# Optimization experiments

Measured on AMD Instinct MI355X. Metric: run time of the kernel, lower is better.

The kernel has to match this reference:

```python
import jax, jax.numpy as jnp
import numpy as np

HIDDEN = 2048
NUM_HEADS = 16
HEAD_DIM = 128
WINDOW_SIZE = 512
NUM_GLOBAL = 16
SCALING = HEAD_DIM ** -0.5


def setup_inputs() -> dict:
    key = jax.random.key(0)
    ks = jax.random.split(key, 5)
    std = HIDDEN ** -0.5
    hidden_states = jax.random.normal(ks[0], (1, 4096, HIDDEN), dtype=jnp.float32)
    # Linear weights stored as (in, out) so y = x @ W
    Wq = jax.random.normal(ks[1], (HIDDEN, NUM_HEADS * HEAD_DIM), dtype=jnp.float32) * std
    Wk = jax.random.normal(ks[2], (HIDDEN, NUM_HEADS * HEAD_DIM), dtype=jnp.float32) * std
    Wv = jax.random.normal(ks[3], (HIDDEN, NUM_HEADS * HEAD_DIM), dtype=jnp.float32) * std
    Wo = jax.random.normal(ks[4], (NUM_HEADS * HEAD_DIM, HIDDEN), dtype=jnp.float32) * std
    return {"hidden_states": hidden_states, "Wq": Wq, "Wk": Wk, "Wv": Wv, "Wo": Wo}


def _sliding_mask(q_len: int, kv_len: int) -> jnp.ndarray:
    q_pos = jnp.arange(q_len)[:, None]
    kv_pos = jnp.arange(kv_len)[None, :]
    half_window = WINDOW_SIZE // 2
    local = jnp.abs(q_pos - kv_pos) < half_window
    glob = (q_pos < NUM_GLOBAL) | (kv_pos < NUM_GLOBAL)
    mask = local | glob
    return jnp.where(mask, 0.0, -jnp.inf).astype(jnp.float32)


def reference(hidden_states, Wq, Wk, Wv, Wo):
    bsz, q_len, _ = hidden_states.shape
    q = (hidden_states @ Wq).reshape(bsz, q_len, NUM_HEADS, HEAD_DIM).transpose(0, 2, 1, 3)
    k = (hidden_states @ Wk).reshape(bsz, q_len, NUM_HEADS, HEAD_DIM).transpose(0, 2, 1, 3)
    v = (hidden_states @ Wv).reshape(bsz, q_len, NUM_HEADS, HEAD_DIM).transpose(0, 2, 1, 3)
    mask = _sliding_mask(q_len, q_len)[None, None]  # [1,1,S,S]
    scores = jnp.einsum("bhqd,bhkd->bhqk", q, k) * SCALING + mask
    attn = jax.nn.softmax(scores.astype(jnp.float32), axis=-1).astype(q.dtype)
    out = jnp.einsum("bhqk,bhkd->bhqd", attn, v)
    out = out.transpose(0, 2, 1, 3).reshape(bsz, q_len, NUM_HEADS * HEAD_DIM)
    return out @ Wo
```

## Files before the change

### kernel.cpp

```cpp
#include <hip/hip_runtime.h>
#include <stdint.h>

#define SEQ    4096
#define HID    2048
#define NQKV   6144
#define QKW    4096
#define NH     16
#define HD     128
#define SCALE  0.08838834764831845f
#define GQC    32

typedef unsigned short u16;
typedef __attribute__((ext_vector_type(8))) short bf16x8;
typedef __attribute__((ext_vector_type(4))) float f32x4;

__device__ __forceinline__ u16 f2bf(float f) {
  union { float f; unsigned u; } v; v.f = f;
  unsigned r = v.u + 0x7FFFu + ((v.u >> 16) & 1u);
  return (u16)(r >> 16);
}

__device__ __forceinline__ float bf2f(u16 b) {
  union { unsigned u; float f; } c; c.u = ((unsigned)b) << 16; return c.f;
}

__device__ __forceinline__ void async16(const u16* g, u16* l) {
  __builtin_amdgcn_global_load_lds(
      (const __attribute__((address_space(1))) unsigned int*)g,
      (__attribute__((address_space(3))) unsigned int*)l, 16, 0, 0);
}

__global__ __launch_bounds__(256) void cvt_f32_bf16(const float* __restrict__ in,
                                                    u16* __restrict__ out, int n4) {
  int i = blockIdx.x * 256 + threadIdx.x;
  if (i >= n4) return;
  float4 v = ((const float4*)in)[i];
  ushort4 o;
  o.x = f2bf(v.x); o.y = f2bf(v.y); o.z = f2bf(v.z); o.w = f2bf(v.w);
  ((ushort4*)out)[i] = o;
}

__global__ __launch_bounds__(256) void transpose_w4(const float* __restrict__ W0,
                                                    const float* __restrict__ W1,
                                                    const float* __restrict__ W2,
                                                    const float* __restrict__ W3,
                                                    u16* __restrict__ Wcat,
                                                    u16* __restrict__ Wot) {
  __shared__ __align__(16) u16 Ts[64 * 68];
  const int n0 = blockIdx.x * 64;
  const int k0 = blockIdx.y * 64;
  const int z = blockIdx.z;
  const float* W = (z == 0) ? W0 : (z == 1) ? W1 : (z == 2) ? W2 : W3;
  u16* Wt = (z < 3) ? (Wcat + (size_t)z * 2048 * 2048) : Wot;
  const int t = threadIdx.x;
#pragma unroll
  for (int p = 0; p < 4; ++p) {
    int f = (t + p * 256) * 4;
    int r = f >> 6, c = f & 63;
    float4 v = *(const float4*)&W[(size_t)(k0 + r) * 2048 + n0 + c];
    ushort4 o; o.x = f2bf(v.x); o.y = f2bf(v.y); o.z = f2bf(v.z); o.w = f2bf(v.w);
    *(ushort4*)&Ts[r * 68 + c] = o;
  }
  __syncthreads();
#pragma unroll
  for (int p = 0; p < 4; ++p) {
    int g = (t + p * 256) * 4;
    int r = g >> 6, c = g & 63;
    ushort4 o;
    o.x = Ts[(c + 0) * 68 + r];
    o.y = Ts[(c + 1) * 68 + r];
    o.z = Ts[(c + 2) * 68 + r];
    o.w = Ts[(c + 3) * 68 + r];
    *(ushort4*)&Wt[(size_t)(n0 + r) * 2048 + k0 + c] = o;
  }
}

template <typename OutT, bool WVT>
__global__ __launch_bounds__(256) void gemm_bt(const u16* __restrict__ A,
                                               const u16* __restrict__ B,
                                               OutT* __restrict__ C,
                                               u16* __restrict__ VTout,
                                               int K, int ldc) {
  __shared__ __align__(16) u16 As[128 * 32];
  __shared__ __align__(16) u16 Bs[128 * 32];
  const int m0 = blockIdx.y * 128;
  const int n0 = blockIdx.x * 128;
  const int tid = threadIdx.x;
  const int wid = tid >> 6;
  const int lane = tid & 63;
  const int wm = wid & 1, wn = wid >> 1;
  const int l15 = lane & 15, g4 = lane >> 4;

  const int srow = wid * 32 + (lane >> 2);
  const int scol = (lane & 3) * 8;

  f32x4 acc[4][4] = {};

  const u16* pa0 = &A[(size_t)(m0 + srow) * K + scol];
  const u16* pa1 = &A[(size_t)(m0 + srow + 16) * K + scol];
  const u16* pb0 = &B[(size_t)(n0 + srow) * K + scol];
  const u16* pb1 = &B[(size_t)(n0 + srow + 16) * K + scol];
  u16* la0 = &As[(wid * 32) * 32];
  u16* la1 = &As[(wid * 32 + 16) * 32];
  u16* lb0 = &Bs[(wid * 32) * 32];
  u16* lb1 = &Bs[(wid * 32 + 16) * 32];

  for (int kt = 0; kt < K; kt += 32) {
    __syncthreads();
    async16(pa0 + kt, la0);
    async16(pa1 + kt, la1);
    async16(pb0 + kt, lb0);
    async16(pb1 + kt, lb1);
    __syncthreads();
    bf16x8 af[4], bfr[4];
#pragma unroll
    for (int i = 0; i < 4; ++i)
      af[i] = *(const bf16x8*)&As[(wm * 64 + i * 16 + l15) * 32 + g4 * 8];
#pragma unroll
    for (int i = 0; i < 4; ++i)
      bfr[i] = *(const bf16x8*)&Bs[(wn * 64 + i * 16 + l15) * 32 + g4 * 8];
#pragma unroll
    for (int mi = 0; mi < 4; ++mi)
#pragma unroll
      for (int ni = 0; ni < 4; ++ni)
        acc[mi][ni] = __builtin_amdgcn_mfma_f32_16x16x32_bf16(af[mi], bfr[ni], acc[mi][ni], 0, 0, 0);
  }

  if (WVT && n0 >= QKW) {
#pragma unroll
    for (int mi = 0; mi < 4; ++mi)
#pragma unroll
      for (int ni = 0; ni < 4; ++ni) {
        const int nv = n0 - QKW + wn * 64 + ni * 16 + l15;
        const int hh = nv >> 7, dd = nv & 127;
        u16* base = &VTout[((size_t)hh * HD + dd) * SEQ];
        const int mb = m0 + wm * 64 + mi * 16 + g4 * 4;
        u16 pk[4];
#pragma unroll
        for (int r = 0; r < 4; ++r) pk[r] = f2bf(acc[mi][ni][r]);
        *(uint2*)&base[mb] = *(uint2*)pk;
      }
  } else {
#pragma unroll
    for (int mi = 0; mi < 4; ++mi)
#pragma unroll
      for (int ni = 0; ni < 4; ++ni) {
        const int n = n0 + wn * 64 + ni * 16 + l15;
#pragma unroll
        for (int r = 0; r < 4; ++r) {
          const int m = m0 + wm * 64 + mi * 16 + g4 * 4 + r;
          float v = acc[mi][ni][r];
          if constexpr (sizeof(OutT) == 2) {
            C[(size_t)m * ldc + n] = (OutT)f2bf(v);
          } else {
            C[(size_t)m * ldc + n] = v;
          }
        }
      }
  }
}

__global__ __launch_bounds__(256, 2) void attn_kernel(const u16* __restrict__ qk,
                                                      const u16* __restrict__ vt,
                                                      u16* __restrict__ out) {
  __shared__ __align__(16) u16 Ks[64 * 128];
  __shared__ __align__(16) u16 VTs[128 * 64];
  __shared__ __align__(16) u16 Ps[128 * 64];
  const int q0 = blockIdx.x * 128;
  const int h = blockIdx.y;
  const int tid = threadIdx.x;
  const int w = tid >> 6;
  const int lane = tid & 63;
  const int l15 = lane & 15, g4 = lane >> 4, l7 = lane & 7;

  bf16x8 qf[2][4];
#pragma unroll
  for (int qs = 0; qs < 2; ++qs) {
    const u16* qrow = &qk[(size_t)(q0 + w * 32 + qs * 16 + l15) * QKW + h * HD + g4 * 8];
#pragma unroll
    for (int kk = 0; kk < 4; ++kk) qf[qs][kk] = *(const bf16x8*)&qrow[kk * 32];
  }

  float m_run[2] = {-1e30f, -1e30f}, l_run[2] = {0.f, 0.f};
  f32x4 o[2][8] = {};

  int lo = q0 - 255;
  int lo_blk = (lo < 0) ? 0 : (lo >> 6);
  int hi_blk = (q0 + 382) >> 6;
  if (hi_blk > 63) hi_blk = 63;
  const int extra = (lo_blk > 0) ? 1 : 0;
  const int nsteps = hi_blk - lo_blk + 1 + extra;

  for (int step = 0; step < nsteps; ++step) {
    const int kb = (extra && step == 0) ? 0 : (lo_blk + step - extra);
    const int kv0 = kb * 64;
    __syncthreads();
#pragma unroll
    for (int p = 0; p < 4; ++p) {
      const int r = w * 16 + p * 4 + (lane >> 4);
      const u16* src = &qk[(size_t)(kv0 + r) * QKW + 2048 + h * HD + (((lane & 15) ^ (r & 15)) * 8)];
      async16(src, &Ks[(w * 16 + p * 4) * 128]);
    }
#pragma unroll
    for (int p = 0; p < 4; ++p) {
      const int r = w * 32 + p * 8 + (lane >> 3);
      const u16* src = &vt[(size_t)h * (HD * SEQ) + (size_t)r * SEQ + kv0 + (((lane & 7) ^ (r & 7)) * 8)];
      async16(src, &VTs[(w * 32 + p * 8) * 64]);
    }
    __syncthreads();

    f32x4 st[2][4] = {};
#pragma unroll
    for (int kk = 0; kk < 4; ++kk) {
      bf16x8 ak[4];
#pragma unroll
      for (int t4 = 0; t4 < 4; ++t4)
        ak[t4] = *(const bf16x8*)&Ks[(t4 * 16 + l15) * 128 + (((kk * 4 + g4) ^ l15) * 8)];
#pragma unroll
      for (int qs = 0; qs < 2; ++qs)
#pragma unroll
        for (int t4 = 0; t4 < 4; ++t4)
          st[qs][t4] = __builtin_amdgcn_mfma_f32_16x16x32_bf16(ak[t4], qf[qs][kk], st[qs][t4], 0, 0, 0);
    }

#pragma unroll
    for (int qs = 0; qs < 2; ++qs) {
      const int q = q0 + w * 32 + qs * 16 + l15;
      float cmax = -1e30f;
#pragma unroll
      for (int t4 = 0; t4 < 4; ++t4)
#pragma unroll
        for (int r = 0; r < 4; ++r) {
          int kv = kv0 + t4 * 16 + g4 * 4 + r;
          int dq = q - kv; if (dq < 0) dq = -dq;
          bool ok = (dq < 256) || (kv < 16);
          float s = ok ? st[qs][t4][r] * SCALE : -1e30f;
          st[qs][t4][r] = s;
          cmax = fmaxf(cmax, s);
        }
      cmax = fmaxf(cmax, __shfl_xor(cmax, 16, 64));
      cmax = fmaxf(cmax, __shfl_xor(cmax, 32, 64));
      float mnew = fmaxf(m_run[qs], cmax);
      float csum = 0.f;
#pragma unroll
      for (int t4 = 0; t4 < 4; ++t4)
#pragma unroll
        for (int r = 0; r < 4; ++r) {
          float p = __expf(st[qs][t4][r] - mnew);
          st[qs][t4][r] = p;
          csum += p;
        }
      csum += __shfl_xor(csum, 16, 64);
      csum += __shfl_xor(csum, 32, 64);
      float a = __expf(m_run[qs] - mnew);
      m_run[qs] = mnew;
      l_run[qs] = l_run[qs] * a + csum;

#pragma unroll
      for (int t4 = 0; t4 < 4; ++t4) {
        u16 pk[4];
#pragma unroll
        for (int r = 0; r < 4; ++r) pk[r] = f2bf(st[qs][t4][r]);
        int c8 = t4 * 2 + (g4 >> 1);
        *(uint2*)&Ps[(w * 32 + qs * 16 + l15) * 64 + ((c8 ^ l7) * 8) + (g4 & 1) * 4] = *(uint2*)pk;
      }
#pragma unroll
      for (int nt = 0; nt < 8; ++nt)
#pragma unroll
        for (int r = 0; r < 4; ++r) o[qs][nt][r] *= a;
    }

#pragma unroll
    for (int ks = 0; ks < 2; ++ks) {
      bf16x8 ap[2];
#pragma unroll
      for (int qs = 0; qs < 2; ++qs)
        ap[qs] = *(const bf16x8*)&Ps[(w * 32 + qs * 16 + l15) * 64 + (((ks * 4 + g4) ^ l7) * 8)];
#pragma unroll
      for (int nt = 0; nt < 8; ++nt) {
        bf16x8 bv = *(const bf16x8*)&VTs[(nt * 16 + l15) * 64 + (((ks * 4 + g4) ^ l7) * 8)];
#pragma unroll
        for (int qs = 0; qs < 2; ++qs)
          o[qs][nt] = __builtin_amdgcn_mfma_f32_16x16x32_bf16(bv, ap[qs], o[qs][nt], 0, 0, 0);
      }
    }
  }

#pragma unroll
  for (int qs = 0; qs < 2; ++qs) {
    if (q0 + w * 32 + qs * 16 < 16) continue;
    const int q = q0 + w * 32 + qs * 16 + l15;
    const float inv = 1.f / l_run[qs];
#pragma unroll
    for (int nt = 0; nt < 8; ++nt) {
      u16 pk[4];
#pragma unroll
      for (int r = 0; r < 4; ++r) pk[r] = f2bf(o[qs][nt][r] * inv);
      *(uint2*)&out[(size_t)q * HID + h * HD + nt * 16 + g4 * 4] = *(uint2*)pk;
    }
  }
}

__global__ __launch_bounds__(256) void attn_global(const u16* __restrict__ qk,
                                                   const u16* __restrict__ vt,
                                                   float* __restrict__ Opart,
                                                   float* __restrict__ MLpart) {
  __shared__ __align__(16) u16 Ks[64 * 136];
  __shared__ __align__(16) u16 Vs[64 * 136];
  const int chunk = blockIdx.x, h = blockIdx.y;
  const int t = threadIdx.x;
  const int q = t >> 4, dg = t & 15;

  float qr[8];
  {
    bf16x8 v = *(const bf16x8*)&qk[(size_t)q * QKW + h * HD + dg * 8];
#pragma unroll
    for (int j = 0; j < 8; ++j) qr[j] = bf2f((u16)v[j]);
  }
  float m_run = -1e30f, l_run = 0.f, o[8] = {};
  const int kvbase = chunk * (SEQ / GQC);

  for (int st = 0; st < (SEQ / GQC) / 64; ++st) {
    const int kv0 = kvbase + st * 64;
    __syncthreads();
#pragma unroll
    for (int p = 0; p < 4; ++p) {
      int f = (t + p * 256) * 8;
      int r = f >> 7, c = f & 127;
      *(uint4*)&Ks[r * 136 + c] = *(const uint4*)&qk[(size_t)(kv0 + r) * QKW + 2048 + h * HD + c];
    }
#pragma unroll
    for (int p = 0; p < 4; ++p) {
      int id = p * 256 + t;
      int d = id >> 3, c8 = id & 7;
      uint4 v = *(const uint4*)&vt[(size_t)h * (HD * SEQ) + (size_t)d * SEQ + kv0 + c8 * 8];
      const u16* pv16 = (const u16*)&v;
#pragma unroll
      for (int j = 0; j < 8; ++j) Vs[(c8 * 8 + j) * 136 + d] = pv16[j];
    }
    __syncthreads();
    for (int kv = 0; kv < 64; ++kv) {
      bf16x8 kr = *(const bf16x8*)&Ks[kv * 136 + dg * 8];
      float s = 0.f;
#pragma unroll
      for (int j = 0; j < 8; ++j) s += qr[j] * bf2f((u16)kr[j]);
      s += __shfl_xor(s, 1, 64); s += __shfl_xor(s, 2, 64);
      s += __shfl_xor(s, 4, 64); s += __shfl_xor(s, 8, 64);
      s *= SCALE;
      float mnew = fmaxf(m_run, s);
      float alpha = __expf(m_run - mnew);
      float p = __expf(s - mnew);
      m_run = mnew;
      l_run = l_run * alpha + p;
      bf16x8 vr = *(const bf16x8*)&Vs[kv * 136 + dg * 8];
#pragma unroll
      for (int j = 0; j < 8; ++j) o[j] = o[j] * alpha + p * bf2f((u16)vr[j]);
    }
  }
  float* op = &Opart[(((size_t)h * GQC + chunk) * 16 + q) * HD + dg * 8];
#pragma unroll
  for (int j = 0; j < 8; ++j) op[j] = o[j];
  if (dg == 0) {
    float* ml = &MLpart[(((size_t)h * GQC + chunk) * 16 + q) * 2];
    ml[0] = m_run; ml[1] = l_run;
  }
}

__global__ __launch_bounds__(256) void attn_gred(const float* __restrict__ Opart,
                                                 const float* __restrict__ MLpart,
                                                 u16* __restrict__ out) {
  const int h = blockIdx.x;
  const int t = threadIdx.x;
  const int q = t >> 4, dg = t & 15;
  float M = -1e30f;
  for (int c = 0; c < GQC; ++c)
    M = fmaxf(M, MLpart[(((size_t)h * GQC + c) * 16 + q) * 2]);
  float L = 0.f, o[8] = {};
  for (int c = 0; c < GQC; ++c) {
    const float* ml = &MLpart[(((size_t)h * GQC + c) * 16 + q) * 2];
    float e = __expf(ml[0] - M);
    L += e * ml[1];
    const float* op = &Opart[(((size_t)h * GQC + c) * 16 + q) * HD + dg * 8];
#pragma unroll
    for (int j = 0; j < 8; ++j) o[j] += e * op[j];
  }
  float inv = 1.f / L;
  u16 tmp[8];
#pragma unroll
  for (int j = 0; j < 8; ++j) tmp[j] = f2bf(o[j] * inv);
  *(uint4*)&out[(size_t)q * HID + h * HD + dg * 8] = *(uint4*)tmp;
}

extern "C" void kernel_launch(void* const* d_in, const int* in_sizes, int n_in,
                              void* d_out, int out_size, void* d_ws, size_t ws_size,
                              hipStream_t stream) {
  const float* X  = (const float*)d_in[0];
  const float* Wq = (const float*)d_in[1];
  const float* Wk = (const float*)d_in[2];
  const float* Wv = (const float*)d_in[3];
  const float* Wo = (const float*)d_in[4];
  float* out = (float*)d_out;

  char* ws = (char*)d_ws;
  u16* Xbf    = (u16*)(ws);
  u16* Wcat   = (u16*)(ws + (size_t)(16 << 20));
  u16* AttnO  = (u16*)(ws + (size_t)(16 << 20));
  float* Opart  = (float*)(ws + (size_t)(32 << 20));
  float* MLpart = (float*)(ws + (size_t)(36 << 20));
  u16* QK     = (u16*)(ws + (size_t)(40 << 20));
  u16* VT     = (u16*)(ws + (size_t)(72 << 20));
  u16* Wot    = (u16*)(ws + (size_t)(88 << 20));

  cvt_f32_bf16<<<dim3(8192), dim3(256), 0, stream>>>(X, Xbf, (SEQ * HID) / 4);
  transpose_w4<<<dim3(32, 32, 4), 256, 0, stream>>>(Wq, Wk, Wv, Wo, Wcat, Wot);
  gemm_bt<u16, true><<<dim3(48, 32), 256, 0, stream>>>(Xbf, Wcat, QK, VT, HID, QKW);
  attn_global<<<dim3(GQC, NH), 256, 0, stream>>>(QK, VT, Opart, MLpart);
  attn_kernel<<<dim3(SEQ / 128, NH), 256, 0, stream>>>(QK, VT, AttnO);
  attn_gred<<<dim3(NH), 256, 0, stream>>>(Opart, MLpart, AttnO);
  gemm_bt<float, false><<<dim3(16, 32), 256, 0, stream>>>(AttnO, Wot, out, nullptr, HID, HID);
}
```

Before: 431.2 us.

## Merge prep kernels, fuse attention launches with atomic reduction, double K-step in GEMM

```diff
diff --git a/kernel.cpp b/kernel.cpp
--- a/kernel.cpp
+++ b/kernel.cpp
@@ -30,29 +30,33 @@
       (__attribute__((address_space(3))) unsigned int*)l, 16, 0, 0);
 }
 
-__global__ __launch_bounds__(256) void cvt_f32_bf16(const float* __restrict__ in,
-                                                    u16* __restrict__ out, int n4) {
-  int i = blockIdx.x * 256 + threadIdx.x;
-  if (i >= n4) return;
-  float4 v = ((const float4*)in)[i];
-  ushort4 o;
-  o.x = f2bf(v.x); o.y = f2bf(v.y); o.z = f2bf(v.z); o.w = f2bf(v.w);
-  ((ushort4*)out)[i] = o;
-}
-
-__global__ __launch_bounds__(256) void transpose_w4(const float* __restrict__ W0,
-                                                    const float* __restrict__ W1,
-                                                    const float* __restrict__ W2,
-                                                    const float* __restrict__ W3,
-                                                    u16* __restrict__ Wcat,
-                                                    u16* __restrict__ Wot) {
+__global__ __launch_bounds__(256) void prep(const float* __restrict__ X,
+                                            const float* __restrict__ W0,
+                                            const float* __restrict__ W1,
+                                            const float* __restrict__ W2,
+                                            const float* __restrict__ W3,
+                                            u16* __restrict__ Xbf,
+                                            u16* __restrict__ Wcat,
+                                            u16* __restrict__ Wot,
+                                            unsigned* __restrict__ cnt) {
+  const int bx = blockIdx.x;
+  const int t = threadIdx.x;
+  if (bx == 0 && t < NH) cnt[t] = 0u;
+  if (bx < 8192) {
+    int i = bx * 256 + t;
+    float4 v = ((const float4*)X)[i];
+    ushort4 o;
+    o.x = f2bf(v.x); o.y = f2bf(v.y); o.z = f2bf(v.z); o.w = f2bf(v.w);
+    ((ushort4*)Xbf)[i] = o;
+    return;
+  }
   __shared__ __align__(16) u16 Ts[64 * 68];
-  const int n0 = blockIdx.x * 64;
-  const int k0 = blockIdx.y * 64;
-  const int z = blockIdx.z;
+  const int b = bx - 8192;
+  const int z = b >> 10;
+  const int k0 = ((b >> 5) & 31) * 64;
+  const int n0 = (b & 31) * 64;
   const float* W = (z == 0) ? W0 : (z == 1) ? W1 : (z == 2) ? W2 : W3;
   u16* Wt = (z < 3) ? (Wcat + (size_t)z * 2048 * 2048) : Wot;
-  const int t = threadIdx.x;
 #pragma unroll
   for (int p = 0; p < 4; ++p) {
     int f = (t + p * 256) * 4;
@@ -81,8 +85,10 @@
                                                OutT* __restrict__ C,
                                                u16* __restrict__ VTout,
                                                int K, int ldc) {
-  __shared__ __align__(16) u16 As[128 * 32];
-  __shared__ __align__(16) u16 Bs[128 * 32];
+  __shared__ __align__(16) u16 As0[128 * 32];
+  __shared__ __align__(16) u16 As1[128 * 32];
+  __shared__ __align__(16) u16 Bs0[128 * 32];
+  __shared__ __align__(16) u16 Bs1[128 * 32];
   const int m0 = blockIdx.y * 128;
   const int n0 = blockIdx.x * 128;
   const int tid = threadIdx.x;
@@ -100,30 +106,47 @@
   const u16* pa1 = &A[(size_t)(m0 + srow + 16) * K + scol];
   const u16* pb0 = &B[(size_t)(n0 + srow) * K + scol];
   const u16* pb1 = &B[(size_t)(n0 + srow + 16) * K + scol];
-  u16* la0 = &As[(wid * 32) * 32];
-  u16* la1 = &As[(wid * 32 + 16) * 32];
-  u16* lb0 = &Bs[(wid * 32) * 32];
-  u16* lb1 = &Bs[(wid * 32 + 16) * 32];
-
-  for (int kt = 0; kt < K; kt += 32) {
+  const int lo0 = (wid * 32) * 32, lo1 = (wid * 32 + 16) * 32;
+
+  for (int kt = 0; kt < K; kt += 64) {
     __syncthreads();
-    async16(pa0 + kt, la0);
-    async16(pa1 + kt, la1);
-    async16(pb0 + kt, lb0);
-    async16(pb1 + kt, lb1);
+    async16(pa0 + kt, &As0[lo0]);
+    async16(pa1 + kt, &As0[lo1]);
+    async16(pb0 + kt, &Bs0[lo0]);
+    async16(pb1 + kt, &Bs0[lo1]);
+    async16(pa0 + kt + 32, &As1[lo0]);
+    async16(pa1 + kt + 32, &As1[lo1]);
+    async16(pb0 + kt + 32, &Bs1[lo0]);
+    async16(pb1 + kt + 32, &Bs1[lo1]);
     __syncthreads();
-    bf16x8 af[4], bfr[4];
-#pragma unroll
-    for (int i = 0; i < 4; ++i)
-      af[i] = *(const bf16x8*)&As[(wm * 64 + i * 16 + l15) * 32 + g4 * 8];
-#pragma unroll
-    for (int i = 0; i < 4; ++i)
-      bfr[i] = *(const bf16x8*)&Bs[(wn * 64 + i * 16 + l15) * 32 + g4 * 8];
-#pragma unroll
-    for (int mi = 0; mi < 4; ++mi)
-#pragma unroll
-      for (int ni = 0; ni < 4; ++ni)
-        acc[mi][ni] = __builtin_amdgcn_mfma_f32_16x16x32_bf16(af[mi], bfr[ni], acc[mi][ni], 0, 0, 0);
+    {
+      bf16x8 af[4], bfr[4];
+#pragma unroll
+      for (int i = 0; i < 4; ++i)
+        af[i] = *(const bf16x8*)&As0[(wm * 64 + i * 16 + l15) * 32 + g4 * 8];
+#pragma unroll
+      for (int i = 0; i < 4; ++i)
+        bfr[i] = *(const bf16x8*)&Bs0[(wn * 64 + i * 16 + l15) * 32 + g4 * 8];
+#pragma unroll
+      for (int mi = 0; mi < 4; ++mi)
+#pragma unroll
+        for (int ni = 0; ni < 4; ++ni)
+          acc[mi][ni] = __builtin_amdgcn_mfma_f32_16x16x32_bf16(af[mi], bfr[ni], acc[mi][ni], 0, 0, 0);
+    }
+    {
+      bf16x8 af[4], bfr[4];
+#pragma unroll
+      for (int i = 0; i < 4; ++i)
+        af[i] = *(const bf16x8*)&As1[(wm * 64 + i * 16 + l15) * 32 + g4 * 8];
+#pragma unroll
+      for (int i = 0; i < 4; ++i)
+        bfr[i] = *(const bf16x8*)&Bs1[(wn * 64 + i * 16 + l15) * 32 + g4 * 8];
+#pragma unroll
+      for (int mi = 0; mi < 4; ++mi)
+#pragma unroll
+        for (int ni = 0; ni < 4; ++ni)
+          acc[mi][ni] = __builtin_amdgcn_mfma_f32_16x16x32_bf16(af[mi], bfr[ni], acc[mi][ni], 0, 0, 0);
+    }
   }
 
   if (WVT && n0 >= QKW) {
@@ -160,235 +183,243 @@
   }
 }
 
-__global__ __launch_bounds__(256, 2) void attn_kernel(const u16* __restrict__ qk,
-                                                      const u16* __restrict__ vt,
-                                                      u16* __restrict__ out) {
-  __shared__ __align__(16) u16 Ks[64 * 128];
-  __shared__ __align__(16) u16 VTs[128 * 64];
-  __shared__ __align__(16) u16 Ps[128 * 64];
-  const int q0 = blockIdx.x * 128;
+__global__ __launch_bounds__(256, 2) void attn_fused(const u16* __restrict__ qk,
+                                                     const u16* __restrict__ vt,
+                                                     u16* __restrict__ out,
+                                                     float* __restrict__ Opart,
+                                                     float* __restrict__ MLpart,
+                                                     unsigned* __restrict__ cnt) {
+  __shared__ __align__(16) u16 smem[24576];
+  __shared__ unsigned lastflag;
   const int h = blockIdx.y;
   const int tid = threadIdx.x;
-  const int w = tid >> 6;
   const int lane = tid & 63;
-  const int l15 = lane & 15, g4 = lane >> 4, l7 = lane & 7;
-
-  bf16x8 qf[2][4];
-#pragma unroll
-  for (int qs = 0; qs < 2; ++qs) {
-    const u16* qrow = &qk[(size_t)(q0 + w * 32 + qs * 16 + l15) * QKW + h * HD + g4 * 8];
-#pragma unroll
-    for (int kk = 0; kk < 4; ++kk) qf[qs][kk] = *(const bf16x8*)&qrow[kk * 32];
-  }
-
-  float m_run[2] = {-1e30f, -1e30f}, l_run[2] = {0.f, 0.f};
-  f32x4 o[2][8] = {};
-
-  int lo = q0 - 255;
-  int lo_blk = (lo < 0) ? 0 : (lo >> 6);
-  int hi_blk = (q0 + 382) >> 6;
-  if (hi_blk > 63) hi_blk = 63;
-  const int extra = (lo_blk > 0) ? 1 : 0;
-  const int nsteps = hi_blk - lo_blk + 1 + extra;
-
-  for (int step = 0; step < nsteps; ++step) {
-    const int kb = (extra && step == 0) ? 0 : (lo_blk + step - extra);
-    const int kv0 = kb * 64;
+
+  if (blockIdx.x < 32) {
+    u16* Ks  = smem;
+    u16* VTs = smem + 8192;
+    u16* Ps  = smem + 16384;
+    const int q0 = blockIdx.x * 128;
+    const int w = tid >> 6;
+    const int l15 = lane & 15, g4 = lane >> 4, l7 = lane & 7;
+
+    bf16x8 qf[2][4];
+#pragma unroll
+    for (int qs = 0; qs < 2; ++qs) {
+      const u16* qrow = &qk[(size_t)(q0 + w * 32 + qs * 16 + l15) * QKW + h * HD + g4 * 8];
+#pragma unroll
+      for (int kk = 0; kk < 4; ++kk) qf[qs][kk] = *(const bf16x8*)&qrow[kk * 32];
+    }
+
+    float m_run[2] = {-1e30f, -1e30f}, l_run[2] = {0.f, 0.f};
+    f32x4 o[2][8] = {};
+
+    int lo = q0 - 255;
+    int lo_blk = (lo < 0) ? 0 : (lo >> 6);
+    int hi_blk = (q0 + 382) >> 6;
+    if (hi_blk > 63) hi_blk = 63;
+    const int extra = (lo_blk > 0) ? 1 : 0;
+    const int nsteps = hi_blk - lo_blk + 1 + extra;
+
+    for (int step = 0; step < nsteps; ++step) {
+      const int kb = (extra && step == 0) ? 0 : (lo_blk + step - extra);
+      const int kv0 = kb * 64;
+      __syncthreads();
+#pragma unroll
+      for (int p = 0; p < 4; ++p) {
+        const int r = w * 16 + p * 4 + (lane >> 4);
+        const u16* src = &qk[(size_t)(kv0 + r) * QKW + 2048 + h * HD + (((lane & 15) ^ (r & 15)) * 8)];
+        async16(src, &Ks[(w * 16 + p * 4) * 128]);
+      }
+#pragma unroll
+      for (int p = 0; p < 4; ++p) {
+        const int r = w * 32 + p * 8 + (lane >> 3);
+        const u16* src = &vt[(size_t)h * (HD * SEQ) + (size_t)r * SEQ + kv0 + (((lane & 7) ^ (r & 7)) * 8)];
+        async16(src, &VTs[(w * 32 + p * 8) * 64]);
+      }
+      __syncthreads();
+
+      f32x4 st[2][4] = {};
+#pragma unroll
+      for (int kk = 0; kk < 4; ++kk) {
+        bf16x8 ak[4];
+#pragma unroll
+        for (int t4 = 0; t4 < 4; ++t4)
+          ak[t4] = *(const bf16x8*)&Ks[(t4 * 16 + l15) * 128 + (((kk * 4 + g4) ^ l15) * 8)];
+#pragma unroll
+        for (int qs = 0; qs < 2; ++qs)
+#pragma unroll
+          for (int t4 = 0; t4 < 4; ++t4)
+            st[qs][t4] = __builtin_amdgcn_mfma_f32_16x16x32_bf16(ak[t4], qf[qs][kk], st[qs][t4], 0, 0, 0);
+      }
+
+#pragma unroll
+      for (int qs = 0; qs < 2; ++qs) {
+        const int q = q0 + w * 32 + qs * 16 + l15;
+        float cmax = -1e30f;
+#pragma unroll
+        for (int t4 = 0; t4 < 4; ++t4)
+#pragma unroll
+          for (int r = 0; r < 4; ++r) {
+            int kv = kv0 + t4 * 16 + g4 * 4 + r;
+            int dq = q - kv; if (dq < 0) dq = -dq;
+            bool ok = (dq < 256) || (kv < 16);
+            float s = ok ? st[qs][t4][r] * SCALE : -1e30f;
+            st[qs][t4][r] = s;
+            cmax = fmaxf(cmax, s);
+          }
+        cmax = fmaxf(cmax, __shfl_xor(cmax, 16, 64));
+        cmax = fmaxf(cmax, __shfl_xor(cmax, 32, 64));
+        float mnew = fmaxf(m_run[qs], cmax);
+        float csum = 0.f;
+#pragma unroll
+        for (int t4 = 0; t4 < 4; ++t4)
+#pragma unroll
+          for (int r = 0; r < 4; ++r) {
+            float p = __expf(st[qs][t4][r] - mnew);
+            st[qs][t4][r] = p;
+            csum += p;
+          }
+        csum += __shfl_xor(csum, 16, 64);
+        csum += __shfl_xor(csum, 32, 64);
+        float a = __expf(m_run[qs] - mnew);
+        m_run[qs] = mnew;
+        l_run[qs] = l_run[qs] * a + csum;
+
+#pragma unroll
+        for (int t4 = 0; t4 < 4; ++t4) {
+          u16 pk[4];
+#pragma unroll
+          for (int r = 0; r < 4; ++r) pk[r] = f2bf(st[qs][t4][r]);
+          int c8 = t4 * 2 + (g4 >> 1);
+          *(uint2*)&Ps[(w * 32 + qs * 16 + l15) * 64 + ((c8 ^ l7) * 8) + (g4 & 1) * 4] = *(uint2*)pk;
+        }
+#pragma unroll
+        for (int nt = 0; nt < 8; ++nt)
+#pragma unroll
+          for (int r = 0; r < 4; ++r) o[qs][nt][r] *= a;
+      }
+
+#pragma unroll
+      for (int ks = 0; ks < 2; ++ks) {
+        bf16x8 ap[2];
+#pragma unroll
+        for (int qs = 0; qs < 2; ++qs)
+          ap[qs] = *(const bf16x8*)&Ps[(w * 32 + qs * 16 + l15) * 64 + (((ks * 4 + g4) ^ l7) * 8)];
+#pragma unroll
+        for (int nt = 0; nt < 8; ++nt) {
+          bf16x8 bv = *(const bf16x8*)&VTs[(nt * 16 + l15) * 64 + (((ks * 4 + g4) ^ l7) * 8)];
+#pragma unroll
+          for (int qs = 0; qs < 2; ++qs)
+            o[qs][nt] = __builtin_amdgcn_mfma_f32_16x16x32_bf16(bv, ap[qs], o[qs][nt], 0, 0, 0);
+        }
+      }
+    }
+
+#pragma unroll
+    for (int qs = 0; qs < 2; ++qs) {
+      if (q0 + w * 32 + qs * 16 < 16) continue;
+      const int q = q0 + w * 32 + qs * 16 + l15;
+      const float inv = 1.f / l_run[qs];
+#pragma unroll
+      for (int nt = 0; nt < 8; ++nt) {
+        u16 pk[4];
+#pragma unroll
+        for (int r = 0; r < 4; ++r) pk[r] = f2bf(o[qs][nt][r] * inv);
+        *(uint2*)&out[(size_t)q * HID + h * HD + nt * 16 + g4 * 4] = *(uint2*)pk;
+      }
+    }
+    return;
+  }
+
+  {
+    u16* Ks = smem;
+    u16* Vs = smem + 8704;
+    const int chunk = blockIdx.x - 32;
+    const int t = tid;
+    const int q = t >> 4, dg = t & 15;
+
+    float qr[8];
+    {
+      bf16x8 v = *(const bf16x8*)&qk[(size_t)q * QKW + h * HD + dg * 8];
+#pragma unroll
+      for (int j = 0; j < 8; ++j) qr[j] = bf2f((u16)v[j]);
+    }
+    float m_run = -1e30f, l_run = 0.f, o[8] = {};
+    const int kvbase = chunk * (SEQ / GQC);
+
+    for (int st = 0; st < (SEQ / GQC) / 64; ++st) {
+      const int kv0 = kvbase + st * 64;
+      __syncthreads();
+#pragma unroll
+      for (int p = 0; p < 4; ++p) {
+        int f = (t + p * 256) * 8;
+        int r = f >> 7, c = f & 127;
+        *(uint4*)&Ks[r * 136 + c] = *(const uint4*)&qk[(size_t)(kv0 + r) * QKW + 2048 + h * HD + c];
+      }
+#pragma unroll
+      for (int p = 0; p < 4; ++p) {
+        int id = p * 256 + t;
+        int d = id >> 3, c8 = id & 7;
+        uint4 v = *(const uint4*)&vt[(size_t)h * (HD * SEQ) + (size_t)d * SEQ + kv0 + c8 * 8];
+        const u16* pv16 = (const u16*)&v;
+#pragma unroll
+        for (int j = 0; j < 8; ++j) Vs[(c8 * 8 + j) * 136 + d] = pv16[j];
+      }
+      __syncthreads();
+      for (int kv = 0; kv < 64; ++kv) {
+        bf16x8 kr = *(const bf16x8*)&Ks[kv * 136 + dg * 8];
+        float s = 0.f;
+#pragma unroll
+        for (int j = 0; j < 8; ++j) s += qr[j] * bf2f((u16)kr[j]);
+        s += __shfl_xor(s, 1, 64); s += __shfl_xor(s, 2, 64);
+        s += __shfl_xor(s, 4, 64); s += __shfl_xor(s, 8, 64);
+        s *= SCALE;
+        float mnew = fmaxf(m_run, s);
+        float alpha = __expf(m_run - mnew);
+        float p = __expf(s - mnew);
+        m_run = mnew;
+        l_run = l_run * alpha + p;
+        bf16x8 vr = *(const bf16x8*)&Vs[kv * 136 + dg * 8];
+#pragma unroll
+        for (int j = 0; j < 8; ++j) o[j] = o[j] * alpha + p * bf2f((u16)vr[j]);
+      }
+    }
+    float* op = &Opart[(((size_t)h * GQC + chunk) * 16 + q) * HD + dg * 8];
+#pragma unroll
+    for (int j = 0; j < 8; ++j) op[j] = o[j];
+    if (dg == 0) {
+      float* ml = &MLpart[(((size_t)h * GQC + chunk) * 16 + q) * 2];
+      ml[0] = m_run; ml[1] = l_run;
+    }
+
     __syncthreads();
-#pragma unroll
-    for (int p = 0; p < 4; ++p) {
-      const int r = w * 16 + p * 4 + (lane >> 4);
-      const u16* src = &qk[(size_t)(kv0 + r) * QKW + 2048 + h * HD + (((lane & 15) ^ (r & 15)) * 8)];
-      async16(src, &Ks[(w * 16 + p * 4) * 128]);
-    }
-#pragma unroll
-    for (int p = 0; p < 4; ++p) {
-      const int r = w * 32 + p * 8 + (lane >> 3);
-      const u16* src = &vt[(size_t)h * (HD * SEQ) + (size_t)r * SEQ + kv0 + (((lane & 7) ^ (r & 7)) * 8)];
-      async16(src, &VTs[(w * 32 + p * 8) * 64]);
+    if (t == 0) {
+      __threadfence();
+      lastflag = (atomicAdd(&cnt[h], 1u) == GQC - 1) ? 1u : 0u;
     }
     __syncthreads();
-
-    f32x4 st[2][4] = {};
-#pragma unroll
-    for (int kk = 0; kk < 4; ++kk) {
-      bf16x8 ak[4];
-#pragma unroll
-      for (int t4 = 0; t4 < 4; ++t4)
-        ak[t4] = *(const bf16x8*)&Ks[(t4 * 16 + l15) * 128 + (((kk * 4 + g4) ^ l15) * 8)];
-#pragma unroll
-      for (int qs = 0; qs < 2; ++qs)
-#pragma unroll
-        for (int t4 = 0; t4 < 4; ++t4)
-          st[qs][t4] = __builtin_amdgcn_mfma_f32_16x16x32_bf16(ak[t4], qf[qs][kk], st[qs][t4], 0, 0, 0);
-    }
-
-#pragma unroll
-    for (int qs = 0; qs < 2; ++qs) {
-      const int q = q0 + w * 32 + qs * 16 + l15;
-      float cmax = -1e30f;
-#pragma unroll
-      for (int t4 = 0; t4 < 4; ++t4)
-#pragma unroll
-        for (int r = 0; r < 4; ++r) {
-          int kv = kv0 + t4 * 16 + g4 * 4 + r;
-          int dq = q - kv; if (dq < 0) dq = -dq;
-          bool ok = (dq < 256) || (kv < 16);
-          float s = ok ? st[qs][t4][r] * SCALE : -1e30f;
-          st[qs][t4][r] = s;
-          cmax = fmaxf(cmax, s);
-        }
-      cmax = fmaxf(cmax, __shfl_xor(cmax, 16, 64));
-      cmax = fmaxf(cmax, __shfl_xor(cmax, 32, 64));
-      float mnew = fmaxf(m_run[qs], cmax);
-      float csum = 0.f;
-#pragma unroll
-      for (int t4 = 0; t4 < 4; ++t4)
-#pragma unroll
-        for (int r = 0; r < 4; ++r) {
-          float p = __expf(st[qs][t4][r] - mnew);
-          st[qs][t4][r] = p;
-          csum += p;
-        }
-      csum += __shfl_xor(csum, 16, 64);
-      csum += __shfl_xor(csum, 32, 64);
-      float a = __expf(m_run[qs] - mnew);
-      m_run[qs] = mnew;
-      l_run[qs] = l_run[qs] * a + csum;
-
-#pragma unroll
-      for (int t4 = 0; t4 < 4; ++t4) {
-        u16 pk[4];
-#pragma unroll
-        for (int r = 0; r < 4; ++r) pk[r] = f2bf(st[qs][t4][r]);
-        int c8 = t4 * 2 + (g4 >> 1);
-        *(uint2*)&Ps[(w * 32 + qs * 16 + l15) * 64 + ((c8 ^ l7) * 8) + (g4 & 1) * 4] = *(uint2*)pk;
-      }
-#pragma unroll
-      for (int nt = 0; nt < 8; ++nt)
-#pragma unroll
-        for (int r = 0; r < 4; ++r) o[qs][nt][r] *= a;
-    }
-
-#pragma unroll
-    for (int ks = 0; ks < 2; ++ks) {
-      bf16x8 ap[2];
-#pragma unroll
-      for (int qs = 0; qs < 2; ++qs)
-        ap[qs] = *(const bf16x8*)&Ps[(w * 32 + qs * 16 + l15) * 64 + (((ks * 4 + g4) ^ l7) * 8)];
-#pragma unroll
-      for (int nt = 0; nt < 8; ++nt) {
-        bf16x8 bv = *(const bf16x8*)&VTs[(nt * 16 + l15) * 64 + (((ks * 4 + g4) ^ l7) * 8)];
-#pragma unroll
-        for (int qs = 0; qs < 2; ++qs)
-          o[qs][nt] = __builtin_amdgcn_mfma_f32_16x16x32_bf16(bv, ap[qs], o[qs][nt], 0, 0, 0);
-      }
-    }
-  }
-
-#pragma unroll
-  for (int qs = 0; qs < 2; ++qs) {
-    if (q0 + w * 32 + qs * 16 < 16) continue;
-    const int q = q0 + w * 32 + qs * 16 + l15;
-    const float inv = 1.f / l_run[qs];
-#pragma unroll
-    for (int nt = 0; nt < 8; ++nt) {
-      u16 pk[4];
-#pragma unroll
-      for (int r = 0; r < 4; ++r) pk[r] = f2bf(o[qs][nt][r] * inv);
-      *(uint2*)&out[(size_t)q * HID + h * HD + nt * 16 + g4 * 4] = *(uint2*)pk;
-    }
-  }
-}
-
-__global__ __launch_bounds__(256) void attn_global(const u16* __restrict__ qk,
-                                                   const u16* __restrict__ vt,
-                                                   float* __restrict__ Opart,
-                                                   float* __restrict__ MLpart) {
-  __shared__ __align__(16) u16 Ks[64 * 136];
-  __shared__ __align__(16) u16 Vs[64 * 136];
-  const int chunk = blockIdx.x, h = blockIdx.y;
-  const int t = threadIdx.x;
-  const int q = t >> 4, dg = t & 15;
-
-  float qr[8];
-  {
-    bf16x8 v = *(const bf16x8*)&qk[(size_t)q * QKW + h * HD + dg * 8];
-#pragma unroll
-    for (int j = 0; j < 8; ++j) qr[j] = bf2f((u16)v[j]);
-  }
-  float m_run = -1e30f, l_run = 0.f, o[8] = {};
-  const int kvbase = chunk * (SEQ / GQC);
-
-  for (int st = 0; st < (SEQ / GQC) / 64; ++st) {
-    const int kv0 = kvbase + st * 64;
-    __syncthreads();
-#pragma unroll
-    for (int p = 0; p < 4; ++p) {
-      int f = (t + p * 256) * 8;
-      int r = f >> 7, c = f & 127;
-      *(uint4*)&Ks[r * 136 + c] = *(const uint4*)&qk[(size_t)(kv0 + r) * QKW + 2048 + h * HD + c];
-    }
-#pragma unroll
-    for (int p = 0; p < 4; ++p) {
-      int id = p * 256 + t;
-      int d = id >> 3, c8 = id & 7;
-      uint4 v = *(const uint4*)&vt[(size_t)h * (HD * SEQ) + (size_t)d * SEQ + kv0 + c8 * 8];
-      const u16* pv16 = (const u16*)&v;
-#pragma unroll
-      for (int j = 0; j < 8; ++j) Vs[(c8 * 8 + j) * 136 + d] = pv16[j];
-    }
-    __syncthreads();
-    for (int kv = 0; kv < 64; ++kv) {
-      bf16x8 kr = *(const bf16x8*)&Ks[kv * 136 + dg * 8];
-      float s = 0.f;
-#pragma unroll
-      for (int j = 0; j < 8; ++j) s += qr[j] * bf2f((u16)kr[j]);
-      s += __shfl_xor(s, 1, 64); s += __shfl_xor(s, 2, 64);
-      s += __shfl_xor(s, 4, 64); s += __shfl_xor(s, 8, 64);
-      s *= SCALE;
-      float mnew = fmaxf(m_run, s);
-      float alpha = __expf(m_run - mnew);
-      float p = __expf(s - mnew);
-      m_run = mnew;
-      l_run = l_run * alpha + p;
-      bf16x8 vr = *(const bf16x8*)&Vs[kv * 136 + dg * 8];
-#pragma unroll
-      for (int j = 0; j < 8; ++j) o[j] = o[j] * alpha + p * bf2f((u16)vr[j]);
-    }
-  }
-  float* op = &Opart[(((size_t)h * GQC + chunk) * 16 + q) * HD + dg * 8];
-#pragma unroll
-  for (int j = 0; j < 8; ++j) op[j] = o[j];
-  if (dg == 0) {
-    float* ml = &MLpart[(((size_t)h * GQC + chunk) * 16 + q) * 2];
-    ml[0] = m_run; ml[1] = l_run;
-  }
-}
-
-__global__ __launch_bounds__(256) void attn_gred(const float* __restrict__ Opart,
-                                                 const float* __restrict__ MLpart,
-                                                 u16* __restrict__ out) {
-  const int h = blockIdx.x;
-  const int t = threadIdx.x;
-  const int q = t >> 4, dg = t & 15;
-  float M = -1e30f;
-  for (int c = 0; c < GQC; ++c)
-    M = fmaxf(M, MLpart[(((size_t)h * GQC + c) * 16 + q) * 2]);
-  float L = 0.f, o[8] = {};
-  for (int c = 0; c < GQC; ++c) {
-    const float* ml = &MLpart[(((size_t)h * GQC + c) * 16 + q) * 2];
-    float e = __expf(ml[0] - M);
-    L += e * ml[1];
-    const float* op = &Opart[(((size_t)h * GQC + c) * 16 + q) * HD + dg * 8];
-#pragma unroll
-    for (int j = 0; j < 8; ++j) o[j] += e * op[j];
-  }
-  float inv = 1.f / L;
-  u16 tmp[8];
-#pragma unroll
-  for (int j = 0; j < 8; ++j) tmp[j] = f2bf(o[j] * inv);
-  *(uint4*)&out[(size_t)q * HID + h * HD + dg * 8] = *(uint4*)tmp;
+    if (lastflag) {
+      __threadfence();
+      float M = -1e30f;
+      for (int c = 0; c < GQC; ++c)
+        M = fmaxf(M, MLpart[(((size_t)h * GQC + c) * 16 + q) * 2]);
+      float L = 0.f, oo[8] = {};
+      for (int c = 0; c < GQC; ++c) {
+        const float* ml = &MLpart[(((size_t)h * GQC + c) * 16 + q) * 2];
+        float e = __expf(ml[0] - M);
+        L += e * ml[1];
+        const float* opc = &Opart[(((size_t)h * GQC + c) * 16 + q) * HD + dg * 8];
+#pragma unroll
+        for (int j = 0; j < 8; ++j) oo[j] += e * opc[j];
+      }
+      float inv = 1.f / L;
+      u16 tmp[8];
+#pragma unroll
+      for (int j = 0; j < 8; ++j) tmp[j] = f2bf(oo[j] * inv);
+      *(uint4*)&out[(size_t)q * HID + h * HD + dg * 8] = *(uint4*)tmp;
+    }
+  }
 }
 
 extern "C" void kernel_launch(void* const* d_in, const int* in_sizes, int n_in,
@@ -407,15 +438,13 @@
   u16* AttnO  = (u16*)(ws + (size_t)(16 << 20));
   float* Opart  = (float*)(ws + (size_t)(32 << 20));
   float* MLpart = (float*)(ws + (size_t)(36 << 20));
+  unsigned* cnt = (unsigned*)d_out;
   u16* QK     = (u16*)(ws + (size_t)(40 << 20));
   u16* VT     = (u16*)(ws + (size_t)(72 << 20));
   u16* Wot    = (u16*)(ws + (size_t)(88 << 20));
 
-  cvt_f32_bf16<<<dim3(8192), dim3(256), 0, stream>>>(X, Xbf, (SEQ * HID) / 4);
-  transpose_w4<<<dim3(32, 32, 4), 256, 0, stream>>>(Wq, Wk, Wv, Wo, Wcat, Wot);
+  prep<<<dim3(12288), 256, 0, stream>>>(X, Wq, Wk, Wv, Wo, Xbf, Wcat, Wot, cnt);
   gemm_bt<u16, true><<<dim3(48, 32), 256, 0, stream>>>(Xbf, Wcat, QK, VT, HID, QKW);
-  attn_global<<<dim3(GQC, NH), 256, 0, stream>>>(QK, VT, Opart, MLpart);
-  attn_kernel<<<dim3(SEQ / 128, NH), 256, 0, stream>>>(QK, VT, AttnO);
-  attn_gred<<<dim3(NH), 256, 0, stream>>>(Opart, MLpart, AttnO);
+  attn_fused<<<dim3(32 + GQC, NH), 256, 0, stream>>>(QK, VT, AttnO, Opart, MLpart, cnt);
   gemm_bt<float, false><<<dim3(16, 32), 256, 0, stream>>>(AttnO, Wot, out, nullptr, HID, HID);
 }
```

Result: faster. 416.0 us (-3.5%).
